# Kernel tuning notes

Measured on AMD Instinct MI355X. Metric: run time of the kernel, lower is better.

## Reference

```python
import jax, jax.numpy as jnp
import numpy as np

DIM = 1024; DEPTH = 2; DSTATE = 128; HEADDIM = 64; DCONV = 4; EXPAND = 2
DINNER = EXPAND * DIM; NHEADS = DINNER // HEADDIM
CONVCH = DINNER + 2 * DSTATE          # x, B, C channels fed through depthwise conv
DINPROJ = 2 * DINNER + 2 * DSTATE + NHEADS  # z, xBC, dt
VOCAB = 256; EPS = 1e-5
B, T = 2, 1024


def _causal_conv(x, w, b):
    # depthwise causal conv1d: x [B,T,C], w [C,K], b [C]
    K = w.shape[1]
    xp = jnp.pad(x, ((0, 0), (K - 1, 0), (0, 0)))
    y = jnp.broadcast_to(b, x.shape)
    for k in range(K):
        y = y + xp[:, k:k + x.shape[1], :] * w[:, k]
    return y


def _mamba2_layer(h, Wp, cw, cb, dtb, alog, Dd, gw, Wo):
    Bb, Tt, _ = h.shape
    zxbcdt = jnp.einsum('btd,pd->btp', h, Wp)   # [B,T,DINPROJ]
    z = zxbcdt[..., :DINNER]
    xBC = zxbcdt[..., DINNER:DINNER + CONVCH]
    dt_raw = zxbcdt[..., DINNER + CONVCH:]
    xBC = jax.nn.silu(_causal_conv(xBC, cw, cb))
    xs = xBC[..., :DINNER].reshape(Bb, Tt, NHEADS, HEADDIM)
    Bm = xBC[..., DINNER:DINNER + DSTATE]        # [B,T,N] (ngroups=1)
    Cm = xBC[..., DINNER + DSTATE:]              # [B,T,N]
    dt = jax.nn.softplus(dt_raw + dtb)           # [B,T,H]
    dA = jnp.exp(dt * (-jnp.exp(alog)))          # [B,T,H]

    def step(s, inps):
        da_t, dt_t, x_t, b_t, c_t = inps
        dbx = dt_t[:, :, None, None] * x_t[..., None] * b_t[:, None, None, :]
        s = da_t[:, :, None, None] * s + dbx     # [B,H,P,N]
        y = jnp.einsum('bhpn,bn->bhp', s, c_t)
        return s, y

    s0 = jnp.zeros((Bb, NHEADS, HEADDIM, DSTATE), h.dtype)
    seq = (jnp.moveaxis(dA, 1, 0), jnp.moveaxis(dt, 1, 0), jnp.moveaxis(xs, 1, 0),
           jnp.moveaxis(Bm, 1, 0), jnp.moveaxis(Cm, 1, 0))
    _, ys = jax.lax.scan(step, s0, seq)          # ys [T,B,H,P]
    y = jnp.moveaxis(ys, 0, 1) + Dd[:, None] * xs
    y = y.reshape(Bb, Tt, DINNER) * jax.nn.silu(z)   # gated RMSNorm (norm(y*silu(z)))
    y = y * jax.lax.rsqrt(jnp.mean(y * y, -1, keepdims=True) + EPS) * gw
    return jnp.einsum('bti,di->btd', y, Wo)


def setup_inputs() -> dict:
    key = jax.random.key(0)
    ks = jax.random.split(key, 8)
    s = 0.02
    inp = {}
    inp['x'] = jax.random.randint(ks[0], (B, T), 0, VOCAB)
    inp['embed'] = jax.random.normal(ks[1], (VOCAB, DIM)) * s
    inp['in_proj_w'] = jax.random.normal(ks[2], (DEPTH, DINPROJ, DIM)) * s
    inp['conv_w'] = jax.random.normal(ks[3], (DEPTH, CONVCH, DCONV)) * 0.2
    inp['conv_b'] = jnp.zeros((DEPTH, CONVCH))
    # dt_bias so softplus(dt) ~ [1e-3, 1e-1]
    inp['dt_bias'] = jax.random.uniform(ks[4], (DEPTH, NHEADS), minval=-4.6, maxval=-2.0)
    inp['A_log'] = jnp.log(jnp.broadcast_to(jnp.arange(1, NHEADS + 1, dtype=jnp.float32), (DEPTH, NHEADS)))
    inp['D'] = jnp.ones((DEPTH, NHEADS))
    inp['gnorm_w'] = jnp.ones((DEPTH, DINNER))
    inp['out_proj_w'] = jax.random.normal(ks[5], (DEPTH, DIM, DINNER)) * s
    inp['final_norm_w'] = jnp.ones((DIM,))
    return inp


def reference(x, embed, in_proj_w, conv_w, conv_b, dt_bias, A_log, D, gnorm_w, out_proj_w, final_norm_w):
    h = embed[x]                                  # [B,T,DIM]
    for l in range(DEPTH):
        h = h + _mamba2_layer(h, in_proj_w[l], conv_w[l], conv_b[l], dt_bias[l],
                              A_log[l], D[l], gnorm_w[l], out_proj_w[l])
    h = h * jax.lax.rsqrt(jnp.mean(h * h, -1, keepdims=True) + EPS) * final_norm_w
    return jnp.einsum('btd,vd->btv', h, embed)    # tied head -> logits [B,T,256]
```

## Files before the change

### kernel.cpp

```cpp
#include <hip/hip_runtime.h>
#include <hip/hip_bf16.h>

#define BT 2048
#define T_SEQ 1024
#define DIM 1024
#define DINNER 2048
#define DSTATE 128
#define HEADDIM 64
#define NHEADS 32
#define CONVCH 2304
#define DINPROJ 4384
#define EPS_F 1e-5f
#define NCHUNK 16

typedef __bf16 bf16x8 __attribute__((ext_vector_type(8)));
typedef float f32x4 __attribute__((ext_vector_type(4)));

__device__ __forceinline__ float b2f(unsigned short u) {
  union { unsigned int i; float f; } v; v.i = ((unsigned int)u) << 16; return v.f;
}
__device__ __forceinline__ unsigned short f2b(float f) {
  unsigned int x = __float_as_uint(f);
  return (unsigned short)((x + 0x7fffu + ((x >> 16) & 1u)) >> 16);
}

__device__ __forceinline__ void gload_lds16(const void* g, void* l) {
  __builtin_amdgcn_global_load_lds(
      (const __attribute__((address_space(1))) unsigned int*)g,
      (__attribute__((address_space(3))) unsigned int*)l, 16, 0, 0);
}

__global__ void cvt_k(const float* __restrict__ in, unsigned short* __restrict__ out, int n) {
  int i = (blockIdx.x * 256 + threadIdx.x) * 4;
  if (i < n) {
    float4 v = *(const float4*)(in + i);
    out[i + 0] = f2b(v.x);
    out[i + 1] = f2b(v.y);
    out[i + 2] = f2b(v.z);
    out[i + 3] = f2b(v.w);
  }
}

__global__ void embed_k(const int* __restrict__ x, const float* __restrict__ emb,
                        float* __restrict__ h, unsigned short* __restrict__ hb) {
  int t = blockIdx.x;
  int tok = x[t];
  int d = threadIdx.x;
#pragma unroll
  for (int j = 0; j < 4; ++j, d += 256) {
    float v = emb[(size_t)tok * DIM + d];
    h[(size_t)t * DIM + d] = v;
    hb[(size_t)t * DIM + d] = f2b(v);
  }
}

template <int MODE, int TM, int TN>
__global__ __launch_bounds__(256) void gemm_bt(
    const unsigned short* __restrict__ A,
    const unsigned short* __restrict__ Bw,
    int M, int N, int K,
    unsigned short* __restrict__ Cout,
    float* __restrict__ aux,
    unsigned short* __restrict__ aux2) {
  constexpr int FM = TM / 32, FN = TN / 32;
  constexpr int JA = TM / 64, JB = TN / 64;
  constexpr int HA = TM * 32, HB = TN * 32;
  __shared__ __align__(16) unsigned short As[2 * HA];
  __shared__ __align__(16) unsigned short Bs[2 * HB];
  const int tid = threadIdx.x;
  const int lane = tid & 63;
  const int wave = tid >> 6;
  const int m0 = blockIdx.y * TM;
  const int n0 = blockIdx.x * TN;
  const int wm = (wave >> 1) * (TM / 2);
  const int wn = (wave & 1) * (TN / 2);
  const int quad = lane >> 4;
  const int r = lane & 15;

  f32x4 acc[FM][FN];
#pragma unroll
  for (int i = 0; i < FM; ++i)
#pragma unroll
    for (int j = 0; j < FN; ++j) acc[i][j] = f32x4{0.f, 0.f, 0.f, 0.f};

  const int rowt = tid >> 2, colt = (tid & 3) * 8;
  const unsigned short* aG[JA];
  unsigned short* aD[JA];
  const unsigned short* bG[JB];
  unsigned short* bD[JB];
#pragma unroll
  for (int j = 0; j < JA; ++j) {
    aG[j] = A + (size_t)(m0 + rowt + j * 64) * K + colt;
    aD[j] = As + wave * 512 + j * 2048;
  }
#pragma unroll
  for (int j = 0; j < JB; ++j) {
    int rb = n0 + rowt + j * 64; if (rb >= N) rb = N - 1;
    bG[j] = Bw + (size_t)rb * K + colt;
    bD[j] = Bs + wave * 512 + j * 2048;
  }

#pragma unroll
  for (int j = 0; j < JA; ++j) gload_lds16(aG[j], aD[j]);
#pragma unroll
  for (int j = 0; j < JB; ++j) gload_lds16(bG[j], bD[j]);
  __syncthreads();

  int cur = 0;
  for (int k0 = 0; k0 < K; k0 += 32) {
    const int nxt = cur ^ 1;
    if (k0 + 32 < K) {
#pragma unroll
      for (int j = 0; j < JA; ++j) gload_lds16(aG[j] + k0 + 32, aD[j] + nxt * HA);
#pragma unroll
      for (int j = 0; j < JB; ++j) gload_lds16(bG[j] + k0 + 32, bD[j] + nxt * HB);
    }
    const bf16x8* ap = (const bf16x8*)(As + cur * HA);
    const bf16x8* bp = (const bf16x8*)(Bs + cur * HB);
    bf16x8 af[FM], bfr[FN];
#pragma unroll
    for (int mt = 0; mt < FM; ++mt) af[mt] = ap[(wm + mt * 16 + r) * 4 + quad];
#pragma unroll
    for (int nt = 0; nt < FN; ++nt) bfr[nt] = bp[(wn + nt * 16 + r) * 4 + quad];
#pragma unroll
    for (int mt = 0; mt < FM; ++mt)
#pragma unroll
      for (int nt = 0; nt < FN; ++nt)
        acc[mt][nt] = __builtin_amdgcn_mfma_f32_16x16x32_bf16(af[mt], bfr[nt], acc[mt][nt], 0, 0, 0);
    __syncthreads();
    cur = nxt;
  }

#pragma unroll
  for (int mt = 0; mt < FM; ++mt) {
#pragma unroll
    for (int nt = 0; nt < FN; ++nt) {
#pragma unroll
      for (int i = 0; i < 4; ++i) {
        int gm = m0 + wm + mt * 16 + quad * 4 + i;
        int gn = n0 + wn + nt * 16 + r;
        if (gn < N) {
          float v = acc[mt][nt][i];
          if (MODE == 0) {
            Cout[(size_t)gm * N + gn] = f2b(v);
            if (gn >= DINNER + CONVCH)
              aux[(size_t)gm * NHEADS + (gn - (DINNER + CONVCH))] = v;
          } else if (MODE == 1) {
            size_t o = (size_t)gm * N + gn;
            float hnv = aux[o] + v;
            aux[o] = hnv;
            aux2[o] = f2b(hnv);
          } else {
            aux[(size_t)gm * N + gn] = v;
          }
        }
      }
    }
  }
}

__global__ void conv_k(const unsigned short* __restrict__ zx,
                       const float* __restrict__ cw,
                       const float* __restrict__ cb,
                       unsigned short* __restrict__ xbc,
                       unsigned short* __restrict__ bcb,
                       const float* __restrict__ dtraw,
                       const float* __restrict__ dtb,
                       const float* __restrict__ alog,
                       float* __restrict__ dtf,
                       float* __restrict__ lnAf) {
  int t = blockIdx.x;
  int tt = t & (T_SEQ - 1);
  if (threadIdx.x < NHEADS) {
    int h = threadIdx.x;
    float xx = dtraw[t * NHEADS + h] + dtb[h];
    float sp = (xx > 20.f) ? xx : log1pf(expf(xx));
    dtf[t * NHEADS + h] = sp;
    lnAf[t * NHEADS + h] = -sp * expf(alog[h]);
  }
  for (int c = threadIdx.x; c < CONVCH; c += 256) {
    float acc = cb[c];
#pragma unroll
    for (int k = 0; k < 4; ++k) {
      int tp = tt - 3 + k;
      if (tp >= 0)
        acc += b2f(zx[(size_t)(t - 3 + k) * DINPROJ + DINNER + c]) * cw[c * 4 + k];
    }
    float s = acc / (1.f + expf(-acc));
    unsigned short sb = f2b(s);
    xbc[(size_t)t * CONVCH + c] = sb;
    if (c >= DINNER) bcb[(size_t)t * 256 + (c - DINNER)] = sb;
  }
}

__global__ __launch_bounds__(256) void ssd_intra(
    const unsigned short* __restrict__ bcb,
    const unsigned short* __restrict__ xbc,
    const float* __restrict__ dtf, const float* __restrict__ lnAf,
    unsigned short* __restrict__ y1buf, unsigned short* __restrict__ SL,
    float* __restrict__ dtot) {
  const int bi = blockIdx.x;
  const int c = bi & 15;
  const int h = (bi >> 4) & 31;
  const int b = bi >> 9;
  const int tid = threadIdx.x;
  const int w = tid >> 6, l = tid & 63, r = l & 15, quad = l >> 4;
  const size_t tok0 = (size_t)b * T_SEQ + c * 64;

  __shared__ __align__(16) unsigned short BCs[64 * 264];
  __shared__ __align__(16) unsigned short Xrow[64 * 72];
  __shared__ __align__(16) unsigned short XTs[64 * 72];
  __shared__ __align__(16) unsigned short XWs[64 * 72];
  __shared__ __align__(16) unsigned short Ms[64 * 72];
  __shared__ float cumL[64], dtL[64];

#pragma unroll
  for (int i = 0; i < 8; ++i) {
    int idx = tid + i * 256;
    int row = idx >> 5, col = (idx & 31) * 8;
    uint4 v = *(const uint4*)(bcb + (tok0 + row) * 256 + col);
    *(uint4*)(BCs + row * 264 + col) = v;
  }
#pragma unroll
  for (int i = 0; i < 2; ++i) {
    int idx = tid + i * 256;
    int u = idx >> 3, pc = (idx & 7) * 8;
    uint4 v = *(const uint4*)(xbc + (tok0 + u) * CONVCH + h * HEADDIM + pc);
    *(uint4*)(Xrow + u * 72 + pc) = v;
  }
  if (tid < 64) {
    float v = lnAf[(tok0 + tid) * NHEADS + h];
    dtL[tid] = dtf[(tok0 + tid) * NHEADS + h];
#pragma unroll
    for (int off = 1; off < 64; off <<= 1) {
      float u = __shfl_up(v, off, 64);
      if (tid >= off) v += u;
    }
    cumL[tid] = v;
    if (tid == 63) dtot[bi] = expf(v);
  }
  __syncthreads();

  const float cum63 = cumL[63];
#pragma unroll
  for (int i = 0; i < 2; ++i) {
    int idx = tid + i * 256;
    int p = idx >> 3, ug = (idx & 7) * 8;
    unsigned short tA[8], tW[8];
#pragma unroll
    for (int j = 0; j < 8; ++j) {
      unsigned short xv = Xrow[(ug + j) * 72 + p];
      tA[j] = xv;
      float ws = dtL[ug + j] * expf(cum63 - cumL[ug + j]);
      tW[j] = f2b(b2f(xv) * ws);
    }
    *(uint4*)(XTs + p * 72 + ug) = *(uint4*)tA;
    *(uint4*)(XWs + p * 72 + ug) = *(uint4*)tW;
  }

  f32x4 g[4];
#pragma unroll
  for (int nt = 0; nt < 4; ++nt) g[nt] = f32x4{0.f, 0.f, 0.f, 0.f};
#pragma unroll
  for (int kk = 0; kk < 4; ++kk) {
    bf16x8 afr = *(const bf16x8*)(BCs + (w * 16 + r) * 264 + 128 + kk * 32 + quad * 8);
#pragma unroll
    for (int nt = 0; nt < 4; ++nt) {
      bf16x8 bfr = *(const bf16x8*)(BCs + (nt * 16 + r) * 264 + kk * 32 + quad * 8);
      g[nt] = __builtin_amdgcn_mfma_f32_16x16x32_bf16(afr, bfr, g[nt], 0, 0, 0);
    }
  }
#pragma unroll
  for (int nt = 0; nt < 4; ++nt) {
#pragma unroll
    for (int i = 0; i < 4; ++i) {
      int t_ = w * 16 + quad * 4 + i;
      int u_ = nt * 16 + r;
      float wv = (u_ <= t_) ? expf(cumL[t_] - cumL[u_]) * dtL[u_] : 0.f;
      Ms[t_ * 72 + u_] = f2b(g[nt][i] * wv);
    }
  }
  __syncthreads();

  f32x4 y1[4];
#pragma unroll
  for (int nt = 0; nt < 4; ++nt) y1[nt] = f32x4{0.f, 0.f, 0.f, 0.f};
#pragma unroll
  for (int kk = 0; kk < 2; ++kk) {
    bf16x8 afr = *(const bf16x8*)(Ms + (w * 16 + r) * 72 + kk * 32 + quad * 8);
#pragma unroll
    for (int nt = 0; nt < 4; ++nt) {
      bf16x8 bfr = *(const bf16x8*)(XTs + (nt * 16 + r) * 72 + kk * 32 + quad * 8);
      y1[nt] = __builtin_amdgcn_mfma_f32_16x16x32_bf16(afr, bfr, y1[nt], 0, 0, 0);
    }
  }
#pragma unroll
  for (int nt = 0; nt < 4; ++nt)
#pragma unroll
    for (int i = 0; i < 4; ++i) {
      int t_ = w * 16 + quad * 4 + i, p_ = nt * 16 + r;
      y1buf[((size_t)bi * 64 + t_) * 64 + p_] = f2b(y1[nt][i]);
    }

  f32x4 sl[8];
#pragma unroll
  for (int nt = 0; nt < 8; ++nt) sl[nt] = f32x4{0.f, 0.f, 0.f, 0.f};
#pragma unroll
  for (int kk = 0; kk < 2; ++kk) {
    bf16x8 afr = *(const bf16x8*)(XWs + (w * 16 + r) * 72 + kk * 32 + quad * 8);
#pragma unroll
    for (int nt = 0; nt < 8; ++nt) {
      union { bf16x8 v; unsigned short u[8]; } bq;
#pragma unroll
      for (int j = 0; j < 8; ++j)
        bq.u[j] = BCs[(kk * 32 + quad * 8 + j) * 264 + nt * 16 + r];
      sl[nt] = __builtin_amdgcn_mfma_f32_16x16x32_bf16(afr, bq.v, sl[nt], 0, 0, 0);
    }
  }
#pragma unroll
  for (int nt = 0; nt < 8; ++nt)
#pragma unroll
    for (int i = 0; i < 4; ++i) {
      int p_ = w * 16 + quad * 4 + i, n_ = nt * 16 + r;
      SL[((size_t)bi * 64 + p_) * 128 + n_] = f2b(sl[nt][i]);
    }
}

__global__ void ssd_state(unsigned short* __restrict__ SL,
                          const float* __restrict__ dtot) {
  int gidx = blockIdx.x * 256 + threadIdx.x;
  int n4 = (gidx & 31) * 4;
  int p = (gidx >> 5) & 63;
  int bh = gidx >> 11;
  float sx = 0.f, sy = 0.f, sz = 0.f, sw = 0.f;
  for (int c = 0; c < NCHUNK; ++c) {
    size_t off = ((size_t)(bh * 16 + c) * 64 + p) * 128 + n4;
    uint2 lv = *(uint2*)(SL + off);
    float d = dtot[bh * 16 + c];
    uint2 sv;
    sv.x = (unsigned)f2b(sx) | ((unsigned)f2b(sy) << 16);
    sv.y = (unsigned)f2b(sz) | ((unsigned)f2b(sw) << 16);
    *(uint2*)(SL + off) = sv;
    sx = d * sx + b2f(lv.x & 0xffff);
    sy = d * sy + b2f(lv.x >> 16);
    sz = d * sz + b2f(lv.y & 0xffff);
    sw = d * sw + b2f(lv.y >> 16);
  }
}

__global__ __launch_bounds__(256) void ssd_inter(
    const unsigned short* __restrict__ bcb,
    const unsigned short* __restrict__ SL,
    const unsigned short* __restrict__ y1buf,
    const unsigned short* __restrict__ xbc,
    const unsigned short* __restrict__ zx,
    const float* __restrict__ lnAf,
    const float* __restrict__ Dw,
    unsigned short* __restrict__ yg) {
  const int bi = blockIdx.x;
  const int c = bi & 15, h = (bi >> 4) & 31, b = bi >> 9;
  const int tid = threadIdx.x;
  const int w = tid >> 6, l = tid & 63, r = l & 15, quad = l >> 4;
  const size_t tok0 = (size_t)b * T_SEQ + c * 64;

  __shared__ __align__(16) unsigned short Cs[64 * 136];
  __shared__ __align__(16) unsigned short Sp[64 * 136];
  __shared__ __align__(16) float Yf[64 * 68];
  __shared__ float cumL[64];

#pragma unroll
  for (int i = 0; i < 4; ++i) {
    int idx = tid + i * 256;
    int row = idx >> 4, col = (idx & 15) * 8;
    uint4 v = *(const uint4*)(bcb + (tok0 + row) * 256 + 128 + col);
    *(uint4*)(Cs + row * 136 + col) = v;
    uint4 s = *(const uint4*)(SL + ((size_t)bi * 64 + row) * 128 + col);
    *(uint4*)(Sp + row * 136 + col) = s;
  }
  if (tid < 64) {
    float v = lnAf[(tok0 + tid) * NHEADS + h];
#pragma unroll
    for (int off = 1; off < 64; off <<= 1) {
      float u = __shfl_up(v, off, 64);
      if (tid >= off) v += u;
    }
    cumL[tid] = v;
  }
  __syncthreads();

  f32x4 yi[4];
#pragma unroll
  for (int nt = 0; nt < 4; ++nt) yi[nt] = f32x4{0.f, 0.f, 0.f, 0.f};
#pragma unroll
  for (int kk = 0; kk < 4; ++kk) {
    bf16x8 afr = *(const bf16x8*)(Cs + (w * 16 + r) * 136 + kk * 32 + quad * 8);
#pragma unroll
    for (int nt = 0; nt < 4; ++nt) {
      bf16x8 bfr = *(const bf16x8*)(Sp + (nt * 16 + r) * 136 + kk * 32 + quad * 8);
      yi[nt] = __builtin_amdgcn_mfma_f32_16x16x32_bf16(afr, bfr, yi[nt], 0, 0, 0);
    }
  }
#pragma unroll
  for (int nt = 0; nt < 4; ++nt)
#pragma unroll
    for (int i = 0; i < 4; ++i) {
      int t_ = w * 16 + quad * 4 + i, p_ = nt * 16 + r;
      float y1 = b2f(y1buf[((size_t)bi * 64 + t_) * 64 + p_]);
      Yf[t_ * 68 + p_] = y1 + expf(cumL[t_]) * yi[nt][i];
    }
  __syncthreads();

  const float Dh = Dw[h];
  const int t_ = tid >> 2, pg = (tid & 3) * 16;
  const size_t tok = tok0 + t_;
  union { uint4 q[2]; unsigned short u[16]; } xv, zv, ov;
  xv.q[0] = *(const uint4*)(xbc + tok * CONVCH + h * 64 + pg);
  xv.q[1] = *(const uint4*)(xbc + tok * CONVCH + h * 64 + pg + 8);
  zv.q[0] = *(const uint4*)(zx + tok * DINPROJ + h * 64 + pg);
  zv.q[1] = *(const uint4*)(zx + tok * DINPROJ + h * 64 + pg + 8);
#pragma unroll
  for (int j = 0; j < 16; ++j) {
    float y = Yf[t_ * 68 + pg + j] + Dh * b2f(xv.u[j]);
    float zf = b2f(zv.u[j]);
    ov.u[j] = f2b(y * (zf / (1.f + expf(-zf))));
  }
  *(uint4*)(yg + tok * DINNER + h * 64 + pg) = ov.q[0];
  *(uint4*)(yg + tok * DINNER + h * 64 + pg + 8) = ov.q[1];
}

__global__ void rms2048_k(const unsigned short* __restrict__ in,
                          const float* __restrict__ w,
                          unsigned short* __restrict__ out) {
  int t = blockIdx.x;
  int base = threadIdx.x * 8;
  union { uint4 q; unsigned short u[8]; } vv;
  vv.q = *(const uint4*)(in + (size_t)t * DINNER + base);
  float f[8];
  float ss = 0.f;
#pragma unroll
  for (int j = 0; j < 8; ++j) { f[j] = b2f(vv.u[j]); ss += f[j] * f[j]; }
#pragma unroll
  for (int o = 32; o > 0; o >>= 1) ss += __shfl_xor(ss, o, 64);
  __shared__ float red[4];
  if ((threadIdx.x & 63) == 0) red[threadIdx.x >> 6] = ss;
  __syncthreads();
  ss = red[0] + red[1] + red[2] + red[3];
  float scale = rsqrtf(ss * (1.f / DINNER) + EPS_F);
#pragma unroll
  for (int j = 0; j < 8; ++j)
    out[(size_t)t * DINNER + base + j] = f2b(f[j] * scale * w[base + j]);
}

__global__ void rmsfinal_k(const float* __restrict__ hf,
                           const float* __restrict__ w,
                           unsigned short* __restrict__ out) {
  int t = blockIdx.x;
  int base = threadIdx.x * 4;
  float4 v = *(const float4*)(hf + (size_t)t * DIM + base);
  float ss = v.x * v.x + v.y * v.y + v.z * v.z + v.w * v.w;
#pragma unroll
  for (int o = 32; o > 0; o >>= 1) ss += __shfl_xor(ss, o, 64);
  __shared__ float red[4];
  if ((threadIdx.x & 63) == 0) red[threadIdx.x >> 6] = ss;
  __syncthreads();
  ss = red[0] + red[1] + red[2] + red[3];
  float scale = rsqrtf(ss * (1.f / DIM) + EPS_F);
  out[(size_t)t * DIM + base + 0] = f2b(v.x * scale * w[base + 0]);
  out[(size_t)t * DIM + base + 1] = f2b(v.y * scale * w[base + 1]);
  out[(size_t)t * DIM + base + 2] = f2b(v.z * scale * w[base + 2]);
  out[(size_t)t * DIM + base + 3] = f2b(v.w * scale * w[base + 3]);
}

extern "C" void kernel_launch(void* const* d_in, const int* in_sizes, int n_in,
                              void* d_out, int out_size, void* d_ws, size_t ws_size,
                              hipStream_t stream) {
  const int*   x    = (const int*)d_in[0];
  const float* emb  = (const float*)d_in[1];
  const float* Wp   = (const float*)d_in[2];
  const float* cw   = (const float*)d_in[3];
  const float* cb   = (const float*)d_in[4];
  const float* dtb  = (const float*)d_in[5];
  const float* alog = (const float*)d_in[6];
  const float* Dw   = (const float*)d_in[7];
  const float* gw   = (const float*)d_in[8];
  const float* Wo   = (const float*)d_in[9];
  const float* fnw  = (const float*)d_in[10];

  char* w = (char*)d_ws;
  auto alloc = [&](size_t bytes) {
    char* p = w; w += (bytes + 255) & ~(size_t)255; return p;
  };
  float* h_f32          = (float*)alloc((size_t)BT * DIM * 4);
  unsigned short* hb    = (unsigned short*)alloc((size_t)BT * DIM * 2);
  unsigned short* zx    = (unsigned short*)alloc((size_t)BT * DINPROJ * 2);
  float* dtraw          = (float*)alloc((size_t)BT * NHEADS * 4);
  float* dtf            = (float*)alloc((size_t)BT * NHEADS * 4);
  float* lnAf           = (float*)alloc((size_t)BT * NHEADS * 4);
  unsigned short* xbc   = (unsigned short*)alloc((size_t)BT * CONVCH * 2);
  unsigned short* bcb   = (unsigned short*)alloc((size_t)BT * 256 * 2);
  unsigned short* SL    = (unsigned short*)alloc((size_t)1024 * 64 * 128 * 2);
  unsigned short* y1buf = (unsigned short*)alloc((size_t)1024 * 64 * 64 * 2);
  float* dtot           = (float*)alloc((size_t)1024 * 4);
  unsigned short* yg    = (unsigned short*)alloc((size_t)BT * DINNER * 2);
  unsigned short* yn    = (unsigned short*)alloc((size_t)BT * DINNER * 2);
  unsigned short* hn    = (unsigned short*)alloc((size_t)BT * DIM * 2);
  unsigned short* Wp_b  = (unsigned short*)alloc((size_t)2 * DINPROJ * DIM * 2);
  unsigned short* Wo_b  = (unsigned short*)alloc((size_t)2 * DIM * DINNER * 2);
  unsigned short* emb_b = (unsigned short*)alloc((size_t)256 * DIM * 2 + 256);

  {
    int nWp = 2 * DINPROJ * DIM;
    int nWo = 2 * DIM * DINNER;
    int nEm = 256 * DIM;
    cvt_k<<<(nWp / 4 + 255) / 256, 256, 0, stream>>>(Wp, Wp_b, nWp);
    cvt_k<<<(nWo / 4 + 255) / 256, 256, 0, stream>>>(Wo, Wo_b, nWo);
    cvt_k<<<(nEm / 4 + 255) / 256, 256, 0, stream>>>(emb, emb_b, nEm);
  }

  embed_k<<<BT, 256, 0, stream>>>(x, emb, h_f32, hb);

  for (int l = 0; l < 2; ++l) {
    const unsigned short* Wpl = Wp_b + (size_t)l * DINPROJ * DIM;
    const unsigned short* Wol = Wo_b + (size_t)l * DIM * DINNER;
    const float* cwl   = cw + (size_t)l * CONVCH * 4;
    const float* cbl   = cb + (size_t)l * CONVCH;
    const float* dtbl  = dtb + l * NHEADS;
    const float* alogl = alog + l * NHEADS;
    const float* Dwl   = Dw + l * NHEADS;
    const float* gwl   = gw + (size_t)l * DINNER;

    gemm_bt<0, 128, 128><<<dim3(35, 16), 256, 0, stream>>>(hb, Wpl, BT, DINPROJ, DIM, zx, dtraw, nullptr);
    conv_k<<<BT, 256, 0, stream>>>(zx, cwl, cbl, xbc, bcb, dtraw, dtbl, alogl, dtf, lnAf);
    ssd_intra<<<1024, 256, 0, stream>>>(bcb, xbc, dtf, lnAf, y1buf, SL, dtot);
    ssd_state<<<512, 256, 0, stream>>>(SL, dtot);
    ssd_inter<<<1024, 256, 0, stream>>>(bcb, SL, y1buf, xbc, zx, lnAf, Dwl, yg);
    rms2048_k<<<BT, 256, 0, stream>>>(yg, gwl, yn);
    gemm_bt<1, 64, 64><<<dim3(16, 32), 256, 0, stream>>>(yn, Wol, BT, DIM, DINNER, nullptr, h_f32, hb);
  }

  rmsfinal_k<<<BT, 256, 0, stream>>>(h_f32, fnw, hn);
  gemm_bt<2, 64, 64><<<dim3(4, 32), 256, 0, stream>>>(hn, emb_b, BT, 256, DIM,
                                                      nullptr, (float*)d_out, nullptr);
}
```

Before: 386.3 us.

## Deepen GEMM LDS pipeline with swizzled tiles and explicit vmcnt waits

Replaces the double-buffered bf16 GEMM main loop with a 3- or 4-buffer prefetch pipeline that issues loads D tiles ahead. It waits on explicit vmcnt counts and a raw s_barrier instead of __syncthreads. The global-to-LDS column layout is XOR-swizzled by row, with matching swizzled fragment reads, to reduce LDS bank conflicts. MFMA issue priority is raised with s_setprio. The cost is more LDS per block, which may lower occupancy. The hand-written waitvm helper only emits waits for counts 0, 2, 4 and 8, so tile shapes with other counts would silently skip the wait.

```diff
diff --git a/kernel.cpp b/kernel.cpp
--- a/kernel.cpp
+++ b/kernel.cpp
@@ -30,6 +30,20 @@
       (__attribute__((address_space(3))) unsigned int*)l, 16, 0, 0);
 }
 
+template <int N>
+__device__ __forceinline__ void waitvm() {
+  if constexpr (N == 0) asm volatile("s_waitcnt vmcnt(0)" ::: "memory");
+  else if constexpr (N == 2) asm volatile("s_waitcnt vmcnt(2)" ::: "memory");
+  else if constexpr (N == 4) asm volatile("s_waitcnt vmcnt(4)" ::: "memory");
+  else if constexpr (N == 8) asm volatile("s_waitcnt vmcnt(8)" ::: "memory");
+}
+
+__device__ __forceinline__ void block_barrier() {
+  __builtin_amdgcn_sched_barrier(0);
+  __builtin_amdgcn_s_barrier();
+  __builtin_amdgcn_sched_barrier(0);
+}
+
 __global__ void cvt_k(const float* __restrict__ in, unsigned short* __restrict__ out, int n) {
   int i = (blockIdx.x * 256 + threadIdx.x) * 4;
   if (i < n) {
@@ -64,9 +78,12 @@
     unsigned short* __restrict__ aux2) {
   constexpr int FM = TM / 32, FN = TN / 32;
   constexpr int JA = TM / 64, JB = TN / 64;
+  constexpr int L = JA + JB;
+  constexpr int D = (TM >= 128) ? 2 : 3;
+  constexpr int NBUF = D + 1;
   constexpr int HA = TM * 32, HB = TN * 32;
-  __shared__ __align__(16) unsigned short As[2 * HA];
-  __shared__ __align__(16) unsigned short Bs[2 * HB];
+  __shared__ __align__(16) unsigned short As[NBUF * HA];
+  __shared__ __align__(16) unsigned short Bs[NBUF * HB];
   const int tid = threadIdx.x;
   const int lane = tid & 63;
   const int wave = tid >> 6;
@@ -83,7 +100,8 @@
 #pragma unroll
     for (int j = 0; j < FN; ++j) acc[i][j] = f32x4{0.f, 0.f, 0.f, 0.f};
 
-  const int rowt = tid >> 2, colt = (tid & 3) * 8;
+  const int rowt = tid >> 2;
+  const int colt = (((tid & 3) ^ (rowt & 3)) * 8);
   const unsigned short* aG[JA];
   unsigned short* aD[JA];
   const unsigned short* bG[JB];
@@ -100,35 +118,50 @@
     bD[j] = Bs + wave * 512 + j * 2048;
   }
 
-#pragma unroll
-  for (int j = 0; j < JA; ++j) gload_lds16(aG[j], aD[j]);
-#pragma unroll
-  for (int j = 0; j < JB; ++j) gload_lds16(bG[j], bD[j]);
-  __syncthreads();
+  auto stage = [&](int kt, int buf) {
+    const int kof = kt * 32;
+#pragma unroll
+    for (int j = 0; j < JA; ++j) gload_lds16(aG[j] + kof, aD[j] + buf * HA);
+#pragma unroll
+    for (int j = 0; j < JB; ++j) gload_lds16(bG[j] + kof, bD[j] + buf * HB);
+  };
+
+  const int nk = K / 32;
+#pragma unroll
+  for (int p = 0; p < D; ++p) stage(p, p);
+  waitvm<(D - 1) * L>();
+  block_barrier();
 
   int cur = 0;
-  for (int k0 = 0; k0 < K; k0 += 32) {
-    const int nxt = cur ^ 1;
-    if (k0 + 32 < K) {
-#pragma unroll
-      for (int j = 0; j < JA; ++j) gload_lds16(aG[j] + k0 + 32, aD[j] + nxt * HA);
-#pragma unroll
-      for (int j = 0; j < JB; ++j) gload_lds16(bG[j] + k0 + 32, bD[j] + nxt * HB);
+  for (int t = 0; t < nk; ++t) {
+    if (t + D < nk) {
+      const int sbuf = (cur == 0) ? NBUF - 1 : cur - 1;
+      stage(t + D, sbuf);
     }
     const bf16x8* ap = (const bf16x8*)(As + cur * HA);
     const bf16x8* bp = (const bf16x8*)(Bs + cur * HB);
     bf16x8 af[FM], bfr[FN];
 #pragma unroll
-    for (int mt = 0; mt < FM; ++mt) af[mt] = ap[(wm + mt * 16 + r) * 4 + quad];
-#pragma unroll
-    for (int nt = 0; nt < FN; ++nt) bfr[nt] = bp[(wn + nt * 16 + r) * 4 + quad];
+    for (int mt = 0; mt < FM; ++mt)
+      af[mt] = ap[(wm + mt * 16 + r) * 4 + (quad ^ (r & 3))];
+#pragma unroll
+    for (int nt = 0; nt < FN; ++nt)
+      bfr[nt] = bp[(wn + nt * 16 + r) * 4 + (quad ^ (r & 3))];
+    __builtin_amdgcn_s_setprio(1);
 #pragma unroll
     for (int mt = 0; mt < FM; ++mt)
 #pragma unroll
       for (int nt = 0; nt < FN; ++nt)
         acc[mt][nt] = __builtin_amdgcn_mfma_f32_16x16x32_bf16(af[mt], bfr[nt], acc[mt][nt], 0, 0, 0);
-    __syncthreads();
-    cur = nxt;
+    __builtin_amdgcn_s_setprio(0);
+    if (t + 1 < nk) {
+      int rem = nk - 2 - t; if (rem > D - 1) rem = D - 1;
+      if (rem == D - 1) waitvm<(D - 1) * L>();
+      else if (D == 3 && rem == 1) waitvm<L>();
+      else waitvm<0>();
+      block_barrier();
+    }
+    cur = (cur + 1 == NBUF) ? 0 : cur + 1;
   }
 
 #pragma unroll
```

Result: slower. 400.5 us (+3.7%).
